# Optimization experiments

Hardware: AMD Instinct MI355X
Metric: run time of the kernel (lower is better)

Reference implementation:

```python
import jax, jax.numpy as jnp
import numpy as np

N, E, T = 20000, 320000, 4
F_IN, HID, F_OUT = 128, 256, 128
EPS = 1e-5  # torch BatchNorm1d default


def _gcn_layer(x, src, dst, ew, W, b, gamma, beta):
    # gather-scale-scatter: out[dst] += ew_e * x[src]
    msgs = ew[:, :, None] * x[src]                      # (E, T, F)
    agg = jax.ops.segment_sum(msgs, dst, num_segments=N)  # (N, T, F)
    h = jnp.einsum('ntf,fh->nth', agg, W) + b            # (N, T, H)
    # BatchNorm1d over channel dim H (training-mode batch stats over N and T)
    mean = h.mean(axis=(0, 1))
    var = h.var(axis=(0, 1))
    h = (h - mean) * jax.lax.rsqrt(var + EPS) * gamma + beta
    return jax.nn.relu(h)


def setup_inputs() -> dict:
    key = jax.random.key(0)
    ks = jax.random.split(key, 8)
    node_features = jax.random.normal(ks[0], (N, T, F_IN), jnp.float32)
    edge_index = jax.random.randint(ks[1], (2, E), 0, N, dtype=jnp.int32)
    edges_weight = jax.random.uniform(ks[2], (E, T), jnp.float32)
    s0 = 1.0 / np.sqrt(F_IN)
    s1 = 1.0 / np.sqrt(HID)
    W0 = jax.random.uniform(ks[3], (F_IN, HID), jnp.float32, -s0, s0)
    b0 = jax.random.uniform(ks[4], (HID,), jnp.float32, -s0, s0)
    W1 = jax.random.uniform(ks[5], (HID, F_OUT), jnp.float32, -s1, s1)
    b1 = jax.random.uniform(ks[6], (F_OUT,), jnp.float32, -s1, s1)
    g0 = jnp.ones((HID,), jnp.float32)
    be0 = jnp.zeros((HID,), jnp.float32)
    g1 = jnp.ones((F_OUT,), jnp.float32)
    be1 = jnp.zeros((F_OUT,), jnp.float32)
    return {"node_features": node_features, "edge_index": edge_index,
            "edges_weight": edges_weight, "W0": W0, "b0": b0, "g0": g0,
            "be0": be0, "W1": W1, "b1": b1, "g1": g1, "be1": be1}


def reference(node_features, edge_index, edges_weight,
              W0, b0, g0, be0, W1, b1, g1, be1):
    src, dst = edge_index[0], edge_index[1]
    h = _gcn_layer(node_features, src, dst, edges_weight, W0, b0, g0, be0)
    h = _gcn_layer(h, src, dst, edges_weight, W1, b1, g1, be1)
    return h
```

## Files before the change

### kernel.cpp

```cpp
#include <hip/hip_runtime.h>


#define T_DIM 4
#define F_DIM 128
#define HID   256
#define TF    512

__global__ void count_kernel(const int* __restrict__ dst, int E, int* __restrict__ deg) {
    int e = blockIdx.x * blockDim.x + threadIdx.x;
    if (e < E) atomicAdd(&deg[dst[e]], 1);
}

__global__ void scan_kernel(const int* __restrict__ deg, int* __restrict__ row_start,
                            int* __restrict__ cursor, int n) {
    __shared__ int part[1024];
    int tid = threadIdx.x;
    int chunk = (n + 1023) >> 10;
    int begin = tid * chunk;
    if (begin > n) begin = n;
    int end = begin + chunk;
    if (end > n) end = n;
    int s = 0;
    for (int i = begin; i < end; ++i) s += deg[i];
    part[tid] = s;
    __syncthreads();
    for (int off = 1; off < 1024; off <<= 1) {
        int v = (tid >= off) ? part[tid - off] : 0;
        __syncthreads();
        part[tid] += v;
        __syncthreads();
    }
    int excl = (tid == 0) ? 0 : part[tid - 1];
    for (int i = begin; i < end; ++i) {
        row_start[i] = excl;
        cursor[i] = excl;
        excl += deg[i];
    }
    if (tid == 1023) row_start[n] = part[1023];
}

__global__ void fill_kernel(const int* __restrict__ src, const int* __restrict__ dst,
                            const float4* __restrict__ ew, int E,
                            int* __restrict__ cursor, int* __restrict__ esrc,
                            float4* __restrict__ ewr) {
    int e = blockIdx.x * blockDim.x + threadIdx.x;
    if (e < E) {
        int d = dst[e];
        int p = atomicAdd(&cursor[d], 1);
        esrc[p] = src[e];
        ewr[p] = ew[e];
    }
}

__global__ __launch_bounds__(256) void agg_kernel(
        const float4* __restrict__ x4, const float* __restrict__ ewr,
        const int* __restrict__ row_start, const int* __restrict__ esrc,
        float4* __restrict__ out4) {
    const int n = blockIdx.x;
    const int tid = threadIdx.x;
    const int p = tid >> 6;
    const int q = tid & 63;
    const int t = q >> 4;
    const int beg = row_start[n], end = row_start[n + 1];
    float4 accA = make_float4(0.f, 0.f, 0.f, 0.f);
    float4 accB = make_float4(0.f, 0.f, 0.f, 0.f);
    for (int i = beg; i < end; i += 4) {
        const int e = i + p;
        if (e < end) {
            const int s = esrc[e];
            const float4* xr = x4 + (size_t)s * 128;
            const float w = ewr[e * 4 + t];
            float4 va = xr[2 * q], vb = xr[2 * q + 1];
            accA.x = fmaf(w, va.x, accA.x); accA.y = fmaf(w, va.y, accA.y);
            accA.z = fmaf(w, va.z, accA.z); accA.w = fmaf(w, va.w, accA.w);
            accB.x = fmaf(w, vb.x, accB.x); accB.y = fmaf(w, vb.y, accB.y);
            accB.z = fmaf(w, vb.z, accB.z); accB.w = fmaf(w, vb.w, accB.w);
        }
    }
    __shared__ float4 red[3][128];
    if (p) { red[p - 1][2 * q] = accA; red[p - 1][2 * q + 1] = accB; }
    __syncthreads();
    if (p == 0) {
        #pragma unroll
        for (int r = 0; r < 3; ++r) {
            float4 a = red[r][2 * q], b = red[r][2 * q + 1];
            accA.x += a.x; accA.y += a.y; accA.z += a.z; accA.w += a.w;
            accB.x += b.x; accB.y += b.y; accB.z += b.z; accB.w += b.w;
        }
        out4[(size_t)n * 128 + 2 * q] = accA;
        out4[(size_t)n * 128 + 2 * q + 1] = accB;
    }
}

template<int BM, int K, int NC, bool FUSE>
__global__ __launch_bounds__(256, 4) void gemm_kernel(
        const float* __restrict__ A, const float* __restrict__ W,
        const float* __restrict__ scale, const float* __restrict__ shift,
        float* __restrict__ out) {
    constexpr int BN = 128, BK = 32;
    constexpr int RPT = BM / 16;
    constexpr int ASTR = BK + 4;
    __shared__ float Al[BM * ASTR];
    __shared__ float Wl[BK * BN];
    const int tid = threadIdx.x;
    const long rowbase = (long)blockIdx.y * BM;
    const int colbase = blockIdx.x * BN;
    const int trow = tid >> 4;
    const int tcol = tid & 15;

    float acc[RPT][8] = {};

    const int nk = K / BK;
    for (int kb = 0; kb < nk; ++kb) {
        #pragma unroll
        for (int it = 0; it < BM * BK / 1024; ++it) {
            int idx = tid + it * 256;
            int r = idx >> 3, q = idx & 7;
            float4 v = *(const float4*)&A[(rowbase + r) * K + kb * BK + q * 4];
            if (FUSE) {
                int ch = kb * BK + q * 4;
                float4 sc = *(const float4*)&scale[ch];
                float4 sh = *(const float4*)&shift[ch];
                v.x = fmaxf(fmaf(sc.x, v.x, sh.x), 0.f);
                v.y = fmaxf(fmaf(sc.y, v.y, sh.y), 0.f);
                v.z = fmaxf(fmaf(sc.z, v.z, sh.z), 0.f);
                v.w = fmaxf(fmaf(sc.w, v.w, sh.w), 0.f);
            }
            *(float4*)&Al[r * ASTR + q * 4] = v;
        }
        #pragma unroll
        for (int it = 0; it < 4; ++it) {
            int idx = tid + it * 256;
            int k = idx >> 5, c4 = idx & 31;
            *(float4*)&Wl[k * BN + c4 * 4] =
                *(const float4*)&W[(long)(kb * BK + k) * NC + colbase + c4 * 4];
        }
        __syncthreads();

        #pragma unroll
        for (int kk4 = 0; kk4 < BK / 4; ++kk4) {
            float4 a4[RPT];
            #pragma unroll
            for (int i = 0; i < RPT; ++i)
                a4[i] = *(const float4*)&Al[(trow + 16 * i) * ASTR + kk4 * 4];
            #pragma unroll
            for (int q = 0; q < 4; ++q) {
                const int kk = kk4 * 4 + q;
                float w[8];
                *(float4*)&w[0] = *(const float4*)&Wl[kk * BN + tcol * 4];
                *(float4*)&w[4] = *(const float4*)&Wl[kk * BN + 64 + tcol * 4];
                #pragma unroll
                for (int i = 0; i < RPT; ++i) {
                    const float a = (q == 0) ? a4[i].x : (q == 1) ? a4[i].y
                                  : (q == 2) ? a4[i].z : a4[i].w;
                    #pragma unroll
                    for (int j = 0; j < 8; ++j)
                        acc[i][j] = fmaf(a, w[j], acc[i][j]);
                }
            }
        }
        __syncthreads();
    }

    #pragma unroll
    for (int i = 0; i < RPT; ++i) {
        float* op = &out[(rowbase + trow + 16 * i) * NC + colbase + tcol * 4];
        *(float4*)&op[0]  = make_float4(acc[i][0], acc[i][1], acc[i][2], acc[i][3]);
        *(float4*)&op[64] = make_float4(acc[i][4], acc[i][5], acc[i][6], acc[i][7]);
    }
}

template<int C>
__global__ __launch_bounds__(256) void stats_kernel(
        const float* __restrict__ h, int rows,
        float* __restrict__ sums, float* __restrict__ sqs) {
    constexpr int Q = C / 4;
    constexpr int RPB = 256 / Q;
    const int q = threadIdx.x & (Q - 1);
    const int sub = threadIdx.x / Q;
    float4 s = make_float4(0.f, 0.f, 0.f, 0.f);
    float4 s2 = make_float4(0.f, 0.f, 0.f, 0.f);
    for (long r = (long)blockIdx.x * RPB + sub; r < rows; r += (long)gridDim.x * RPB) {
        float4 v = *(const float4*)&h[r * C + q * 4];
        s.x += v.x; s.y += v.y; s.z += v.z; s.w += v.w;
        s2.x = fmaf(v.x, v.x, s2.x); s2.y = fmaf(v.y, v.y, s2.y);
        s2.z = fmaf(v.z, v.z, s2.z); s2.w = fmaf(v.w, v.w, s2.w);
    }
    __shared__ float4 redS[256], redQ[256];
    redS[threadIdx.x] = s;
    redQ[threadIdx.x] = s2;
    __syncthreads();
    if (sub == 0) {
        #pragma unroll
        for (int u = 1; u < RPB; ++u) {
            float4 a = redS[u * Q + q], b = redQ[u * Q + q];
            s.x += a.x; s.y += a.y; s.z += a.z; s.w += a.w;
            s2.x += b.x; s2.y += b.y; s2.z += b.z; s2.w += b.w;
        }
        atomicAdd(&sums[q * 4 + 0], s.x);
        atomicAdd(&sums[q * 4 + 1], s.y);
        atomicAdd(&sums[q * 4 + 2], s.z);
        atomicAdd(&sums[q * 4 + 3], s.w);
        atomicAdd(&sqs[q * 4 + 0], s2.x);
        atomicAdd(&sqs[q * 4 + 1], s2.y);
        atomicAdd(&sqs[q * 4 + 2], s2.z);
        atomicAdd(&sqs[q * 4 + 3], s2.w);
    }
}

__global__ void finalize_kernel(const float* __restrict__ sums, const float* __restrict__ sqs,
                                const float* __restrict__ g, const float* __restrict__ be,
                                float* __restrict__ scale, float* __restrict__ shift,
                                int C, float invR) {
    int c = threadIdx.x;
    if (c < C) {
        float mean = sums[c] * invR;
        float var = sqs[c] * invR - mean * mean;
        float a = g[c] * rsqrtf(var + 1e-5f);
        scale[c] = a;
        shift[c] = fmaf(-mean, a, be[c]);
    }
}

__global__ void bnapply_kernel(const float4* __restrict__ h4,
                               const float* __restrict__ scale, const float* __restrict__ shift,
                               float4* __restrict__ out4, int n4) {
    int i = blockIdx.x * 256 + threadIdx.x;
    if (i >= n4) return;
    float4 v = h4[i];
    int cb = (i & 31) << 2;
    float4 sc = *(const float4*)&scale[cb];
    float4 sh = *(const float4*)&shift[cb];
    v.x = fmaxf(fmaf(sc.x, v.x, sh.x), 0.f);
    v.y = fmaxf(fmaf(sc.y, v.y, sh.y), 0.f);
    v.z = fmaxf(fmaf(sc.z, v.z, sh.z), 0.f);
    v.w = fmaxf(fmaf(sc.w, v.w, sh.w), 0.f);
    out4[i] = v;
}

extern "C" void kernel_launch(void* const* d_in, const int* in_sizes, int n_in,
                              void* d_out, int out_size, void* d_ws, size_t ws_size,
                              hipStream_t stream) {
    const float* x   = (const float*)d_in[0];
    const int*   ei  = (const int*)d_in[1];
    const float* ew  = (const float*)d_in[2];
    const float* W0  = (const float*)d_in[3];
    const float* g0  = (const float*)d_in[5];
    const float* be0 = (const float*)d_in[6];
    const float* W1  = (const float*)d_in[7];
    const float* g1  = (const float*)d_in[9];
    const float* be1 = (const float*)d_in[10];
    float* out = (float*)d_out;

    const int N = in_sizes[0] / TF;
    const int E = in_sizes[1] / 2;
    const int ROWS = N * T_DIM;

    const int* src = ei;
    const int* dst = ei + E;

    float* h1   = (float*)d_ws;
    float* bufC = h1 + (size_t)ROWS * HID;
    float* h2   = bufC + (size_t)ROWS * F_DIM;
    int* deg       = (int*)(h2 + (size_t)ROWS * F_DIM);
    int* row_start = deg + N;
    int* cursor    = row_start + N + 1;
    int* esrc      = cursor + N + 1;
    float* ewr     = (float*)(esrc + E);
    float* sums0   = ewr + (size_t)E * 4;
    float* sqs0    = sums0 + HID;
    float* sums1   = sqs0 + HID;
    float* sqs1    = sums1 + F_DIM;
    float* scale0  = sqs1 + F_DIM;
    float* shift0  = scale0 + HID;
    float* scale1  = shift0 + HID;
    float* shift1  = scale1 + F_DIM;

    hipMemsetAsync(deg, 0, N * sizeof(int), stream);
    hipMemsetAsync(sums0, 0, (2 * HID + 2 * F_DIM) * sizeof(float), stream);

    const int eb = (E + 255) / 256;
    count_kernel<<<eb, 256, 0, stream>>>(dst, E, deg);
    scan_kernel<<<1, 1024, 0, stream>>>(deg, row_start, cursor, N);
    fill_kernel<<<eb, 256, 0, stream>>>(src, dst, (const float4*)ew, E, cursor,
                                        esrc, (float4*)ewr);

    agg_kernel<<<N, 256, 0, stream>>>((const float4*)x, ewr, row_start, esrc,
                                      (float4*)bufC);
    gemm_kernel<128, 128, 256, false><<<dim3(2, ROWS / 128), 256, 0, stream>>>(
        bufC, W0, nullptr, nullptr, h1);
    stats_kernel<256><<<256, 256, 0, stream>>>(h1, ROWS, sums0, sqs0);
    finalize_kernel<<<1, 256, 0, stream>>>(sums0, sqs0, g0, be0, scale0, shift0, HID,
                                           1.f / (float)ROWS);

    gemm_kernel<64, 256, 128, true><<<dim3(1, ROWS / 64), 256, 0, stream>>>(
        h1, W1, scale0, shift0, bufC);
    agg_kernel<<<N, 256, 0, stream>>>((const float4*)bufC, ewr, row_start, esrc,
                                      (float4*)h2);
    stats_kernel<128><<<256, 256, 0, stream>>>(h2, ROWS, sums1, sqs1);
    finalize_kernel<<<1, 128, 0, stream>>>(sums1, sqs1, g1, be1, scale1, shift1, F_DIM,
                                           1.f / (float)ROWS);
    bnapply_kernel<<<(ROWS * F_DIM / 4 + 255) / 256, 256, 0, stream>>>(
        (const float4*)h2, scale1, shift1, (float4*)out, ROWS * F_DIM / 4);
}
```

Before: 614.2 us.

## Replace FP32 SIMT GEMMs with split-bf16 MFMA GEMMs using direct LDS loads

Both dense GEMMs move from scalar FP32 FMA loops to MFMA 16x16x32 bf16 instructions. Each operand is split into high and low bf16 halves, and three MFMA products (hi*hi, hi*lo, lo*hi) approximate FP32 accuracy. The first aggregation now writes the split bf16 activations directly, and the weights are pre-split and transposed by a new small kernel on every call. Tiles go into LDS through global_load_lds with an XOR swizzle. This adds extra launches and conversion work, and accuracy depends on the 3-term split.

Measured after the change: 536.5 us. -12.6%, faster.

```diff
diff --git a/kernel.cpp b/kernel.cpp
--- a/kernel.cpp
+++ b/kernel.cpp
@@ -5,6 +5,24 @@
 #define F_DIM 128
 #define HID   256
 #define TF    512
+
+typedef __attribute__((ext_vector_type(8))) short bf16x8;
+typedef __attribute__((ext_vector_type(4))) float f32x4;
+
+__device__ __forceinline__ ushort f2bf(float x) {
+    union { float f; unsigned u; } v; v.f = x;
+    unsigned r = v.u + 0x7FFF + ((v.u >> 16) & 1);
+    return (ushort)(r >> 16);
+}
+__device__ __forceinline__ float bf2f(ushort b) {
+    union { float f; unsigned u; } v; v.u = ((unsigned)b) << 16;
+    return v.f;
+}
+__device__ __forceinline__ void gl_lds16(const void* gsrc, void* ldst) {
+    __builtin_amdgcn_global_load_lds(
+        (const __attribute__((address_space(1))) unsigned*)gsrc,
+        (__attribute__((address_space(3))) unsigned*)ldst, 16, 0, 0);
+}
 
 __global__ void count_kernel(const int* __restrict__ dst, int E, int* __restrict__ deg) {
     int e = blockIdx.x * blockDim.x + threadIdx.x;
@@ -16,10 +34,8 @@
     __shared__ int part[1024];
     int tid = threadIdx.x;
     int chunk = (n + 1023) >> 10;
-    int begin = tid * chunk;
-    if (begin > n) begin = n;
-    int end = begin + chunk;
-    if (end > n) end = n;
+    int begin = tid * chunk; if (begin > n) begin = n;
+    int end = begin + chunk; if (end > n) end = n;
     int s = 0;
     for (int i = begin; i < end; ++i) s += deg[i];
     part[tid] = s;
@@ -32,9 +48,7 @@
     }
     int excl = (tid == 0) ? 0 : part[tid - 1];
     for (int i = begin; i < end; ++i) {
-        row_start[i] = excl;
-        cursor[i] = excl;
-        excl += deg[i];
+        row_start[i] = excl; cursor[i] = excl; excl += deg[i];
     }
     if (tid == 1023) row_start[n] = part[1023];
 }
@@ -52,10 +66,22 @@
     }
 }
 
+__global__ void wsplit_kernel(const float* __restrict__ W, int K, int NC,
+                              ushort* __restrict__ hi, ushort* __restrict__ lo) {
+    int idx = blockIdx.x * 256 + threadIdx.x;
+    if (idx >= K * NC) return;
+    int k = idx / NC, c = idx % NC;
+    float x = W[idx];
+    ushort h = f2bf(x);
+    hi[(size_t)c * K + k] = h;
+    lo[(size_t)c * K + k] = f2bf(x - bf2f(h));
+}
+
+template<bool BF16OUT>
 __global__ __launch_bounds__(256) void agg_kernel(
         const float4* __restrict__ x4, const float* __restrict__ ewr,
         const int* __restrict__ row_start, const int* __restrict__ esrc,
-        float4* __restrict__ out4) {
+        float4* __restrict__ out4, ushort* __restrict__ ohi, ushort* __restrict__ olo) {
     const int n = blockIdx.x;
     const int tid = threadIdx.x;
     const int p = tid >> 6;
@@ -87,86 +113,138 @@
             accA.x += a.x; accA.y += a.y; accA.z += a.z; accA.w += a.w;
             accB.x += b.x; accB.y += b.y; accB.z += b.z; accB.w += b.w;
         }
-        out4[(size_t)n * 128 + 2 * q] = accA;
-        out4[(size_t)n * 128 + 2 * q + 1] = accB;
+        if (BF16OUT) {
+            float v[8] = {accA.x, accA.y, accA.z, accA.w, accB.x, accB.y, accB.z, accB.w};
+            uint4 hw, lw;
+            unsigned hu[4], lu[4];
+            #pragma unroll
+            for (int j = 0; j < 4; ++j) {
+                ushort h0 = f2bf(v[2 * j]), h1 = f2bf(v[2 * j + 1]);
+                ushort l0 = f2bf(v[2 * j] - bf2f(h0)), l1 = f2bf(v[2 * j + 1] - bf2f(h1));
+                hu[j] = (unsigned)h0 | ((unsigned)h1 << 16);
+                lu[j] = (unsigned)l0 | ((unsigned)l1 << 16);
+            }
+            hw.x = hu[0]; hw.y = hu[1]; hw.z = hu[2]; hw.w = hu[3];
+            lw.x = lu[0]; lw.y = lu[1]; lw.z = lu[2]; lw.w = lu[3];
+            *(uint4*)&ohi[(size_t)n * TF + q * 8] = hw;
+            *(uint4*)&olo[(size_t)n * TF + q * 8] = lw;
+        } else {
+            out4[(size_t)n * 128 + 2 * q] = accA;
+            out4[(size_t)n * 128 + 2 * q + 1] = accB;
+        }
     }
 }
 
 template<int BM, int K, int NC, bool FUSE>
-__global__ __launch_bounds__(256, 4) void gemm_kernel(
-        const float* __restrict__ A, const float* __restrict__ W,
+__global__ __launch_bounds__(256, 4) void gemm_mfma(
+        const ushort* __restrict__ A_hi, const ushort* __restrict__ A_lo,
+        const float* __restrict__ Af32,
+        const ushort* __restrict__ Wt_hi, const ushort* __restrict__ Wt_lo,
         const float* __restrict__ scale, const float* __restrict__ shift,
         float* __restrict__ out) {
-    constexpr int BN = 128, BK = 32;
-    constexpr int RPT = BM / 16;
-    constexpr int ASTR = BK + 4;
-    __shared__ float Al[BM * ASTR];
-    __shared__ float Wl[BK * BN];
+    constexpr int BN = 128;
+    constexpr int MT = BM / 64;
+    __shared__ __align__(16) unsigned char AsH[BM * 64], AsL[BM * 64];
+    __shared__ __align__(16) unsigned char WsH[BN * 64], WsL[BN * 64];
     const int tid = threadIdx.x;
+    const int w = tid >> 6, l = tid & 63;
     const long rowbase = (long)blockIdx.y * BM;
     const int colbase = blockIdx.x * BN;
-    const int trow = tid >> 4;
-    const int tcol = tid & 15;
-
-    float acc[RPT][8] = {};
-
-    const int nk = K / BK;
-    for (int kb = 0; kb < nk; ++kb) {
-        #pragma unroll
-        for (int it = 0; it < BM * BK / 1024; ++it) {
-            int idx = tid + it * 256;
-            int r = idx >> 3, q = idx & 7;
-            float4 v = *(const float4*)&A[(rowbase + r) * K + kb * BK + q * 4];
-            if (FUSE) {
-                int ch = kb * BK + q * 4;
+
+    f32x4 acc[MT][8];
+    #pragma unroll
+    for (int mt = 0; mt < MT; ++mt)
+        #pragma unroll
+        for (int nt = 0; nt < 8; ++nt) acc[mt][nt] = (f32x4){0.f, 0.f, 0.f, 0.f};
+
+    for (int kb = 0; kb < K / 32; ++kb) {
+        if (kb) __syncthreads();
+        {
+            const int b = l & 3;
+            #pragma unroll
+            for (int cc = 0; cc < 2; ++cc) {
+                int c = 2 * w + cc;
+                int cl = c * 16 + (l >> 2);
+                size_t go = (size_t)(colbase + cl) * K + kb * 32 + ((b ^ (cl & 3)) << 3);
+                gl_lds16(Wt_hi + go, WsH + c * 1024);
+                gl_lds16(Wt_lo + go, WsL + c * 1024);
+            }
+        }
+        if (!FUSE) {
+            const int b = l & 3;
+            #pragma unroll
+            for (int cc = 0; cc < BM / 64; ++cc) {
+                int c = w * (BM / 64) + cc;
+                int r = c * 16 + (l >> 2);
+                size_t go = (size_t)(rowbase + r) * K + kb * 32 + ((b ^ (r & 3)) << 3);
+                gl_lds16(A_hi + go, AsH + c * 1024);
+                gl_lds16(A_lo + go, AsL + c * 1024);
+            }
+        } else {
+            #pragma unroll
+            for (int p = 0; p < BM * 32 / 1024; ++p) {
+                int idx = p * 256 + tid;
+                int r = idx >> 3, k4 = idx & 7;
+                float4 v = *(const float4*)&Af32[(rowbase + r) * K + kb * 32 + k4 * 4];
+                int ch = kb * 32 + k4 * 4;
                 float4 sc = *(const float4*)&scale[ch];
                 float4 sh = *(const float4*)&shift[ch];
                 v.x = fmaxf(fmaf(sc.x, v.x, sh.x), 0.f);
                 v.y = fmaxf(fmaf(sc.y, v.y, sh.y), 0.f);
                 v.z = fmaxf(fmaf(sc.z, v.z, sh.z), 0.f);
                 v.w = fmaxf(fmaf(sc.w, v.w, sh.w), 0.f);
-            }
-            *(float4*)&Al[r * ASTR + q * 4] = v;
-        }
-        #pragma unroll
-        for (int it = 0; it < 4; ++it) {
-            int idx = tid + it * 256;
-            int k = idx >> 5, c4 = idx & 31;
-            *(float4*)&Wl[k * BN + c4 * 4] =
-                *(const float4*)&W[(long)(kb * BK + k) * NC + colbase + c4 * 4];
+                ushort h[4], lo[4];
+                float vv[4] = {v.x, v.y, v.z, v.w};
+                #pragma unroll
+                for (int j = 0; j < 4; ++j) {
+                    h[j] = f2bf(vv[j]);
+                    lo[j] = f2bf(vv[j] - bf2f(h[j]));
+                }
+                unsigned long long hq = (unsigned long long)((unsigned)h[0] | ((unsigned)h[1] << 16))
+                                      | ((unsigned long long)((unsigned)h[2] | ((unsigned)h[3] << 16)) << 32);
+                unsigned long long lq = (unsigned long long)((unsigned)lo[0] | ((unsigned)lo[1] << 16))
+                                      | ((unsigned long long)((unsigned)lo[2] | ((unsigned)lo[3] << 16)) << 32);
+                int off = r * 64 + (((k4 >> 1) ^ (r & 3)) << 4) + (k4 & 1) * 8;
+                *(unsigned long long*)(AsH + off) = hq;
+                *(unsigned long long*)(AsL + off) = lq;
+            }
         }
         __syncthreads();
 
-        #pragma unroll
-        for (int kk4 = 0; kk4 < BK / 4; ++kk4) {
-            float4 a4[RPT];
-            #pragma unroll
-            for (int i = 0; i < RPT; ++i)
-                a4[i] = *(const float4*)&Al[(trow + 16 * i) * ASTR + kk4 * 4];
-            #pragma unroll
-            for (int q = 0; q < 4; ++q) {
-                const int kk = kk4 * 4 + q;
-                float w[8];
-                *(float4*)&w[0] = *(const float4*)&Wl[kk * BN + tcol * 4];
-                *(float4*)&w[4] = *(const float4*)&Wl[kk * BN + 64 + tcol * 4];
-                #pragma unroll
-                for (int i = 0; i < RPT; ++i) {
-                    const float a = (q == 0) ? a4[i].x : (q == 1) ? a4[i].y
-                                  : (q == 2) ? a4[i].z : a4[i].w;
-                    #pragma unroll
-                    for (int j = 0; j < 8; ++j)
-                        acc[i][j] = fmaf(a, w[j], acc[i][j]);
-                }
-            }
-        }
-        __syncthreads();
+        const int g = l >> 4;
+        bf16x8 ah[MT], al[MT];
+        #pragma unroll
+        for (int mt = 0; mt < MT; ++mt) {
+            int ar = w * 16 * MT + mt * 16 + (l & 15);
+            int off = ar * 64 + ((g ^ (ar & 3)) << 4);
+            ah[mt] = *(const bf16x8*)(AsH + off);
+            al[mt] = *(const bf16x8*)(AsL + off);
+        }
+        #pragma unroll
+        for (int nt = 0; nt < 8; ++nt) {
+            int bc = nt * 16 + (l & 15);
+            int off = bc * 64 + ((g ^ (bc & 3)) << 4);
+            bf16x8 bh = *(const bf16x8*)(WsH + off);
+            bf16x8 bl = *(const bf16x8*)(WsL + off);
+            #pragma unroll
+            for (int mt = 0; mt < MT; ++mt) {
+                acc[mt][nt] = __builtin_amdgcn_mfma_f32_16x16x32_bf16(ah[mt], bh, acc[mt][nt], 0, 0, 0);
+                acc[mt][nt] = __builtin_amdgcn_mfma_f32_16x16x32_bf16(ah[mt], bl, acc[mt][nt], 0, 0, 0);
+                acc[mt][nt] = __builtin_amdgcn_mfma_f32_16x16x32_bf16(al[mt], bh, acc[mt][nt], 0, 0, 0);
+            }
+        }
     }
 
     #pragma unroll
-    for (int i = 0; i < RPT; ++i) {
-        float* op = &out[(rowbase + trow + 16 * i) * NC + colbase + tcol * 4];
-        *(float4*)&op[0]  = make_float4(acc[i][0], acc[i][1], acc[i][2], acc[i][3]);
-        *(float4*)&op[64] = make_float4(acc[i][4], acc[i][5], acc[i][6], acc[i][7]);
+    for (int mt = 0; mt < MT; ++mt) {
+        long r0 = rowbase + w * 16 * MT + mt * 16 + (l >> 4) * 4;
+        #pragma unroll
+        for (int nt = 0; nt < 8; ++nt) {
+            int c = colbase + nt * 16 + (l & 15);
+            #pragma unroll
+            for (int j = 0; j < 4; ++j)
+                out[(size_t)(r0 + j) * NC + c] = acc[mt][nt][j];
+        }
     }
 }
 
@@ -187,8 +265,7 @@
         s2.z = fmaf(v.z, v.z, s2.z); s2.w = fmaf(v.w, v.w, s2.w);
     }
     __shared__ float4 redS[256], redQ[256];
-    redS[threadIdx.x] = s;
-    redQ[threadIdx.x] = s2;
+    redS[threadIdx.x] = s; redQ[threadIdx.x] = s2;
     __syncthreads();
     if (sub == 0) {
         #pragma unroll
@@ -197,14 +274,10 @@
             s.x += a.x; s.y += a.y; s.z += a.z; s.w += a.w;
             s2.x += b.x; s2.y += b.y; s2.z += b.z; s2.w += b.w;
         }
-        atomicAdd(&sums[q * 4 + 0], s.x);
-        atomicAdd(&sums[q * 4 + 1], s.y);
-        atomicAdd(&sums[q * 4 + 2], s.z);
-        atomicAdd(&sums[q * 4 + 3], s.w);
-        atomicAdd(&sqs[q * 4 + 0], s2.x);
-        atomicAdd(&sqs[q * 4 + 1], s2.y);
-        atomicAdd(&sqs[q * 4 + 2], s2.z);
-        atomicAdd(&sqs[q * 4 + 3], s2.w);
+        atomicAdd(&sums[q * 4 + 0], s.x); atomicAdd(&sums[q * 4 + 1], s.y);
+        atomicAdd(&sums[q * 4 + 2], s.z); atomicAdd(&sums[q * 4 + 3], s.w);
+        atomicAdd(&sqs[q * 4 + 0], s2.x); atomicAdd(&sqs[q * 4 + 1], s2.y);
+        atomicAdd(&sqs[q * 4 + 2], s2.z); atomicAdd(&sqs[q * 4 + 3], s2.w);
     }
 }
 
@@ -259,13 +332,15 @@
     const int* src = ei;
     const int* dst = ei + E;
 
-    float* h1   = (float*)d_ws;
-    float* bufC = h1 + (size_t)ROWS * HID;
-    float* h2   = bufC + (size_t)ROWS * F_DIM;
+    float* h1  = (float*)d_ws;
+    float* y2  = h1 + (size_t)ROWS * HID;
+    float* h2  = y2 + (size_t)ROWS * F_DIM;
+    ushort* A1h = (ushort*)h2;
+    ushort* A1l = A1h + (size_t)ROWS * F_DIM;
     int* deg       = (int*)(h2 + (size_t)ROWS * F_DIM);
     int* row_start = deg + N;
     int* cursor    = row_start + N + 1;
-    int* esrc      = cursor + N + 1;
+    int* esrc      = cursor + N + 3;
     float* ewr     = (float*)(esrc + E);
     float* sums0   = ewr + (size_t)E * 4;
     float* sqs0    = sums0 + HID;
@@ -275,6 +350,10 @@
     float* shift0  = scale0 + HID;
     float* scale1  = shift0 + HID;
     float* shift1  = scale1 + F_DIM;
+    ushort* Wt0h   = (ushort*)(shift1 + F_DIM);
+    ushort* Wt0l   = Wt0h + 256 * 128;
+    ushort* Wt1h   = Wt0l + 256 * 128;
+    ushort* Wt1l   = Wt1h + 128 * 256;
 
     hipMemsetAsync(deg, 0, N * sizeof(int), stream);
     hipMemsetAsync(sums0, 0, (2 * HID + 2 * F_DIM) * sizeof(float), stream);
@@ -284,19 +363,21 @@
     scan_kernel<<<1, 1024, 0, stream>>>(deg, row_start, cursor, N);
     fill_kernel<<<eb, 256, 0, stream>>>(src, dst, (const float4*)ew, E, cursor,
                                         esrc, (float4*)ewr);
-
-    agg_kernel<<<N, 256, 0, stream>>>((const float4*)x, ewr, row_start, esrc,
-                                      (float4*)bufC);
-    gemm_kernel<128, 128, 256, false><<<dim3(2, ROWS / 128), 256, 0, stream>>>(
-        bufC, W0, nullptr, nullptr, h1);
+    wsplit_kernel<<<128, 256, 0, stream>>>(W0, 128, 256, Wt0h, Wt0l);
+    wsplit_kernel<<<128, 256, 0, stream>>>(W1, 256, 128, Wt1h, Wt1l);
+
+    agg_kernel<true><<<N, 256, 0, stream>>>((const float4*)x, ewr, row_start, esrc,
+                                            nullptr, A1h, A1l);
+    gemm_mfma<128, 128, 256, false><<<dim3(2, ROWS / 128), 256, 0, stream>>>(
+        A1h, A1l, nullptr, Wt0h, Wt0l, nullptr, nullptr, h1);
     stats_kernel<256><<<256, 256, 0, stream>>>(h1, ROWS, sums0, sqs0);
     finalize_kernel<<<1, 256, 0, stream>>>(sums0, sqs0, g0, be0, scale0, shift0, HID,
                                            1.f / (float)ROWS);
 
-    gemm_kernel<64, 256, 128, true><<<dim3(1, ROWS / 64), 256, 0, stream>>>(
-        h1, W1, scale0, shift0, bufC);
-    agg_kernel<<<N, 256, 0, stream>>>((const float4*)bufC, ewr, row_start, esrc,
-                                      (float4*)h2);
+    gemm_mfma<64, 256, 128, true><<<dim3(1, ROWS / 64), 256, 0, stream>>>(
+        nullptr, nullptr, h1, Wt1h, Wt1l, scale0, shift0, y2);
+    agg_kernel<false><<<N, 256, 0, stream>>>((const float4*)y2, ewr, row_start, esrc,
+                                             (float4*)h2, nullptr, nullptr);
     stats_kernel<128><<<256, 256, 0, stream>>>(h2, ROWS, sums1, sqs1);
     finalize_kernel<<<1, 128, 0, stream>>>(sums1, sqs1, g1, be1, scale1, shift1, F_DIM,
                                            1.f / (float)ROWS);
```
